# Performance work log

Measured on AMD Instinct MI355X. Metric: run time of the kernel, lower is better.

The kernel has to match this reference:

```python
import jax, jax.numpy as jnp
import numpy as np

WINDOW = (7, 7, 7)
DIM = 192
HEADS = 6
B_ = 256
NW = 32
N = int(np.prod(WINDOW))


def _relative_position_index(window_size):
    coords = np.stack(np.meshgrid(*[np.arange(w) for w in window_size], indexing='ij'))
    cf = coords.reshape(len(window_size), -1)  # (3, N)
    rel = cf[:, :, None] - cf[:, None, :]      # (3, N, N)
    rel = rel.transpose(1, 2, 0).copy()        # (N, N, 3)
    for i, w in enumerate(window_size):
        rel[:, :, i] += w - 1
    rel[:, :, 0] *= (2 * window_size[1] - 1) * (2 * window_size[2] - 1)
    rel[:, :, 1] *= 2 * window_size[2] - 1
    return rel.sum(-1).astype(np.int32)       # (N, N)


def setup_inputs() -> dict:
    key = jax.random.key(0)
    ks = jax.random.split(key, 8)
    table_rows = int(np.prod([2 * w - 1 for w in WINDOW]))  # 2197
    s = 0.02
    return {
        'skip': jax.random.normal(ks[0], (B_, N, DIM), jnp.float32),
        'x_up': jax.random.normal(ks[1], (B_, N, DIM), jnp.float32),
        'mask': jax.random.normal(ks[2], (NW, N, N), jnp.float32),
        'rel_index': jnp.asarray(_relative_position_index(WINDOW)),
        'table': s * jax.random.normal(ks[3], (table_rows, HEADS), jnp.float32),
        'kv_w': jax.random.normal(ks[4], (DIM, 2 * DIM), jnp.float32) / np.sqrt(DIM),
        'kv_b': jnp.zeros((2 * DIM,), jnp.float32),
        'proj_w': jax.random.normal(ks[5], (DIM, DIM), jnp.float32) / np.sqrt(DIM),
        'proj_b': jnp.zeros((DIM,), jnp.float32),
    }


def reference(skip, x_up, mask, rel_index, table, kv_w, kv_b, proj_w, proj_b):
    B, n, C = skip.shape
    H = HEADS
    D = C // H
    scale = D ** -0.5
    # kv projection: (B, N, 2C) -> k, v each (B, H, N, D)
    kv = skip @ kv_w + kv_b
    kv = kv.reshape(B, n, 2, H, D)
    k = kv[:, :, 0].transpose(0, 2, 1, 3)
    v = kv[:, :, 1].transpose(0, 2, 1, 3)
    q = (x_up.reshape(B, n, H, D).transpose(0, 2, 1, 3)) * scale
    attn = jnp.einsum('bhnd,bhmd->bhnm', q, k)  # (B, H, N, N)
    # gathered relative position bias: (N, N, H) -> (H, N, N)
    bias = table[rel_index].transpose(2, 0, 1)
    attn = attn + bias[None]
    nW = mask.shape[0]
    attn = attn.reshape(B // nW, nW, H, n, n) + mask[None, :, None]
    attn = jax.nn.softmax(attn.reshape(B, H, n, n), axis=-1)
    x = jnp.einsum('bhnm,bhmd->bhnd', attn, v)
    x = x.transpose(0, 2, 1, 3).reshape(B, n, C)
    return x @ proj_w + proj_b
```

## Files before the change

kernel.cpp:

```cpp
#include <hip/hip_runtime.h>
#include <hip/hip_bf16.h>

#define B_  256
#define N_  343
#define C_  192
#define H_  6
#define D_  32
#define NW_ 32
#define NN_ (N_*N_)
#define TROWS 2197
#define NP_ 352
#define PLANE (NP_*NP_)

typedef unsigned int  uint32;
typedef unsigned short u16;
typedef __attribute__((ext_vector_type(8))) short bf16x8;
typedef __attribute__((ext_vector_type(4))) float f32x4;

union frag8 { uint4 u4; bf16x8 h8; short s[8]; };

__device__ __forceinline__ float bf2f(u16 u){
  union { uint32 u; float f; } v; v.u = ((uint32)u) << 16; return v.f;
}
__device__ __forceinline__ u16 f2bf(float f){
  union { float f; uint32 u; } v; v.f = f;
  uint32 u = v.u;
  return (u16)((u + 0x7FFFu + ((u >> 16) & 1u)) >> 16);
}

__device__ __forceinline__ bool detect_f32(const uint32* w){
  int c = 0;
  #pragma unroll
  for (int u = 0; u < 32; u++){
    int e = (w[u*37] >> 7) & 0xFF;
    c += (e > 150);
  }
  return c >= 3;
}
__device__ __forceinline__ float ldf(const void* p, size_t i, bool f32){
  return f32 ? ((const float*)p)[i] : bf2f(((const u16*)p)[i]);
}
__device__ __forceinline__ void stf(void* p, size_t i, float v, bool f32){
  if (f32) ((float*)p)[i] = v;
  else     ((u16*)p)[i]   = f2bf(v);
}

__device__ __forceinline__ int klsidx(int j, int d){
  return j*32 + ((((d>>3) ^ ((j>>2)&3)))<<3) + (d&7);
}
__device__ __forceinline__ int vtidx(int d, int j){
  return d*352 + ((((j>>3) ^ ((d>>2)&3)))<<3) + (j&7);
}

__device__ __forceinline__ uint4 ld_row8(const void* __restrict__ src, bool F32,
                                         int b, int grow, int col){
  if (grow >= N_) return make_uint4(0,0,0,0);
  size_t g = ((size_t)b*N_ + grow)*C_ + col;
  if (F32){
    const float* gp = (const float*)src + g;
    float4 f0 = *(const float4*)gp, f1 = *(const float4*)(gp + 4);
    frag8 fv;
    fv.s[0]=(short)f2bf(f0.x); fv.s[1]=(short)f2bf(f0.y);
    fv.s[2]=(short)f2bf(f0.z); fv.s[3]=(short)f2bf(f0.w);
    fv.s[4]=(short)f2bf(f1.x); fv.s[5]=(short)f2bf(f1.y);
    fv.s[6]=(short)f2bf(f1.z); fv.s[7]=(short)f2bf(f1.w);
    return fv.u4;
  }
  return *(const uint4*)((const u16*)src + g);
}


__global__ void prep_bp(const void* __restrict__ skip, const int* __restrict__ rel,
                        const void* __restrict__ table, u16* __restrict__ bp){
  const bool F32 = detect_f32((const uint32*)skip);
  size_t gid = ((size_t)blockIdx.x*256 + threadIdx.x)*8;
  int p   = (int)(gid / PLANE);
  int rem = (int)(gid % PLANE);
  int i = rem / NP_, j0 = rem % NP_;
  frag8 o;
  #pragma unroll
  for (int m = 0; m < 8; m++){
    int j = j0 + m; float v = 0.f;
    if (i < N_ && j < N_){
      int r = rel[i*N_ + j];
      v = ldf(table, (size_t)r*H_ + p, F32);
    }
    o.s[m] = (short)f2bf(v);
  }
  *(uint4*)&bp[gid] = o.u4;
}

__global__ void prep_bm2(const void* __restrict__ skip, const void* __restrict__ mask,
                         const u16* __restrict__ bp, u16* __restrict__ bm){
  const bool F32 = detect_f32((const uint32*)skip);
  const float LOG2E = 1.4426950408889634f;
  size_t gid = ((size_t)blockIdx.x*256 + threadIdx.x)*8;
  int pl  = (int)(gid / PLANE);
  int rem = (int)(gid % PLANE);
  int i = rem / NP_, j0 = rem % NP_;
  int w = pl / H_, h = pl % H_;
  frag8 bg; bg.u4 = *(const uint4*)&bp[(size_t)h*PLANE + rem];
  frag8 o;
  #pragma unroll
  for (int m = 0; m < 8; m++){
    int j = j0 + m;
    float v = bf2f((u16)bg.s[m]);
    if (i < N_ && j < N_) v += ldf(mask, (size_t)w*NN_ + (size_t)i*N_ + j, F32);
    o.s[m] = (short)f2bf(v * LOG2E);
  }
  *(uint4*)&bm[gid] = o.u4;
}

__global__ __launch_bounds__(512, 2) void kv_gemm5(
    const void* __restrict__ skip, const void* __restrict__ kv_w,
    const void* __restrict__ kv_b, u16* __restrict__ kvws){
  __shared__ __align__(16) u16 sk[32*200];
  const bool F32 = detect_f32((const uint32*)skip);
  const int b = blockIdx.x;
  const int t = threadIdx.x, lane = t & 63, wave = t >> 6;
  const int n16 = lane & 15, q = lane >> 4;

  float kvb[3];
  u16*  p3[3];
  int   d3[3], isK[3];
  frag8 bw[3][6];
  #pragma unroll
  for (int c3 = 0; c3 < 3; c3++){
    int col = (wave*3 + c3)*16 + n16;
    kvb[c3] = ldf(kv_b, col, F32);
    #pragma unroll
    for (int ks = 0; ks < 6; ks++)
      #pragma unroll
      for (int j = 0; j < 8; j++)
        bw[c3][ks].s[j] = (short)f2bf(ldf(kv_w, (size_t)(ks*32 + q*8 + j)*384 + col, F32));
    if (col < 192){
      int h = col >> 5; d3[c3] = col & 31; isK[c3] = 1;
      p3[c3] = kvws + (size_t)(b*H_ + h)*22528;
    } else {
      int cv = col - 192; int h = cv >> 5; d3[c3] = cv & 31; isK[c3] = 0;
      p3[c3] = kvws + (size_t)(b*H_ + h)*22528 + 11264;
    }
  }

  const int r0 = t/24,        c0 = (t%24)*8;
  const int r1 = (t+512)/24,  c1 = ((t+512)%24)*8;
  const bool two = (t < 256);
  uint4 pre0 = ld_row8(skip, F32, b, r0, c0);
  uint4 pre1 = two ? ld_row8(skip, F32, b, r1, c1) : make_uint4(0,0,0,0);

  for (int rc = 0; rc < 11; rc++){
    __syncthreads();
    *(uint4*)&sk[r0*200 + c0] = pre0;
    if (two) *(uint4*)&sk[r1*200 + c1] = pre1;
    __syncthreads();
    if (rc < 10){
      int rb = (rc+1)*32;
      pre0 = ld_row8(skip, F32, b, rb + r0, c0);
      if (two) pre1 = ld_row8(skip, F32, b, rb + r1, c1);
    }
    frag8 af[2][6];
    #pragma unroll
    for (int half = 0; half < 2; half++)
      #pragma unroll
      for (int ks = 0; ks < 6; ks++)
        af[half][ks].u4 = *(const uint4*)&sk[(half*16 + n16)*200 + ks*32 + q*8];
    #pragma unroll
    for (int c3 = 0; c3 < 3; c3++){
      #pragma unroll
      for (int half = 0; half < 2; half++){
        f32x4 acc = {0.f,0.f,0.f,0.f};
        #pragma unroll
        for (int ks = 0; ks < 6; ks++)
          acc = __builtin_amdgcn_mfma_f32_16x16x32_bf16(af[half][ks].h8, bw[c3][ks].h8, acc, 0,0,0);
        #pragma unroll
        for (int r = 0; r < 4; r++){
          int grow = rc*32 + half*16 + q*4 + r;
          u16 val = f2bf(acc[r] + kvb[c3]);
          if (isK[c3]) p3[c3][klsidx(grow, d3[c3])] = val;
          else         p3[c3][vtidx(d3[c3], grow)] = val;
        }
      }
    }
  }
}

#define A2_VT  11264
#define A2_TOT 22528

__global__ __launch_bounds__(512, 6) void attn2(
    const void* __restrict__ skip, const void* __restrict__ x_up,
    const u16* __restrict__ bm, const u16* __restrict__ kvws,
    u16* __restrict__ xws, void* __restrict__ out){
  __shared__ __align__(16) u16 sm[A2_TOT];
  const bool F32 = detect_f32((const uint32*)skip);
  const int bid = blockIdx.x;
  const int b = bid / H_, h = bid % H_;
  const int w = b & (NW_-1);
  const int t = threadIdx.x, lane = t & 63, wave = t >> 6;
  const int n16 = lane & 15, q = lane >> 4;

  {
    const uint4* src = (const uint4*)(kvws + (size_t)bid*22528);
    uint4* dst = (uint4*)sm;
    for (int u = t; u < 2816; u += 512) dst[u] = src[u];
  }
  __syncthreads();

  const u16* bmp = bm + (size_t)(w*H_ + h)*PLANE;
  const float SC2 = 0.17677669529663687f * 1.4426950408889634f;

  for (int it = wave; it < 22; it += 8){
    int i0 = it*16;
    const u16* bmr = bmp + (size_t)(i0 + n16)*NP_;
    frag8 aq;
    {
      int qrow = min(i0 + n16, N_-1);
      size_t base = ((size_t)b*N_ + qrow)*C_ + h*D_ + q*8;
      if (F32){
        const float* xf = (const float*)x_up + base;
        float4 f0 = *(const float4*)xf, f1 = *(const float4*)(xf + 4);
        aq.s[0]=(short)f2bf(f0.x); aq.s[1]=(short)f2bf(f0.y);
        aq.s[2]=(short)f2bf(f0.z); aq.s[3]=(short)f2bf(f0.w);
        aq.s[4]=(short)f2bf(f1.x); aq.s[5]=(short)f2bf(f1.y);
        aq.s[6]=(short)f2bf(f1.z); aq.s[7]=(short)f2bf(f1.w);
      } else {
        aq.u4 = *(const uint4*)((const u16*)x_up + base);
      }
    }
    f32x4 O0 = {0.f,0.f,0.f,0.f}, O1 = {0.f,0.f,0.f,0.f};
    float lp = 0.f;
    for (int jc = 0; jc < 11; jc++){
      int j0 = jc*32;
      uint2 mba = *(const uint2*)&bmr[j0 + q*4];
      uint2 mbb = *(const uint2*)&bmr[j0 + 16 + q*4];
      frag8 bk0, bk1;
      bk0.u4 = *(const uint4*)&sm[klsidx(j0 + n16, q*8)];
      bk1.u4 = *(const uint4*)&sm[klsidx(j0 + 16 + n16, q*8)];
      f32x4 z = {0.f,0.f,0.f,0.f};
      f32x4 s0 = __builtin_amdgcn_mfma_f32_16x16x32_bf16(bk0.h8, aq.h8, z, 0,0,0);
      f32x4 s1 = __builtin_amdgcn_mfma_f32_16x16x32_bf16(bk1.h8, aq.h8, z, 0,0,0);
      union { uint2 v; u16 e[4]; } Ua, Ub;
      Ua.v = mba; Ub.v = mbb;
      float pa[4], pb[4];
      #pragma unroll
      for (int r = 0; r < 4; r++){
        pa[r] = exp2f(fmaf(s0[r], SC2, bf2f(Ua.e[r])));
        float eb = exp2f(fmaf(s1[r], SC2, bf2f(Ub.e[r])));
        pb[r] = (j0 + 16 + q*4 + r < N_) ? eb : 0.f;
        lp += pa[r] + pb[r];
      }
      uint32 A0, A1, B0, B1;
      asm("v_cvt_pk_bf16_f32 %0, %1, %2" : "=v"(A0) : "v"(pa[0]), "v"(pa[1]));
      asm("v_cvt_pk_bf16_f32 %0, %1, %2" : "=v"(A1) : "v"(pa[2]), "v"(pa[3]));
      asm("v_cvt_pk_bf16_f32 %0, %1, %2" : "=v"(B0) : "v"(pb[0]), "v"(pb[1]));
      asm("v_cvt_pk_bf16_f32 %0, %1, %2" : "=v"(B1) : "v"(pb[2]), "v"(pb[3]));
      int src0 = ((q & 1) << 5) + n16;
      int src1 = src0 + 16;
      uint32 a0s = (uint32)__shfl((int)A0, src0), a1s = (uint32)__shfl((int)A1, src0);
      uint32 a2s = (uint32)__shfl((int)A0, src1), a3s = (uint32)__shfl((int)A1, src1);
      uint32 b0s = (uint32)__shfl((int)B0, src0), b1s = (uint32)__shfl((int)B1, src0);
      uint32 b2s = (uint32)__shfl((int)B0, src1), b3s = (uint32)__shfl((int)B1, src1);
      bool lo = (q < 2);
      frag8 ap;
      ap.u4.x = lo ? a0s : b0s;
      ap.u4.y = lo ? a1s : b1s;
      ap.u4.z = lo ? a2s : b2s;
      ap.u4.w = lo ? a3s : b3s;
      frag8 bv0, bv1;
      bv0.u4 = *(const uint4*)&sm[A2_VT + vtidx(n16,      j0 + q*8)];
      bv1.u4 = *(const uint4*)&sm[A2_VT + vtidx(16 + n16, j0 + q*8)];
      O0 = __builtin_amdgcn_mfma_f32_16x16x32_bf16(ap.h8, bv0.h8, O0, 0,0,0);
      O1 = __builtin_amdgcn_mfma_f32_16x16x32_bf16(ap.h8, bv1.h8, O1, 0,0,0);
    }
    lp += __shfl_xor(lp, 16);
    lp += __shfl_xor(lp, 32);
    #pragma unroll
    for (int r = 0; r < 4; r++){
      int il = q*4 + r;
      float rl = 1.f / __shfl(lp, (lane & 48) | il);
      int i = i0 + il;
      if (i < N_){
        if (xws){
          u16* xp = xws + ((size_t)(b*H_ + h)*N_ + i)*D_;
          xp[n16]      = f2bf(O0[r]*rl);
          xp[16 + n16] = f2bf(O1[r]*rl);
        } else {
          size_t ob = ((size_t)b*N_ + i)*C_ + h*D_;
          stf(out, ob + n16,      O0[r]*rl, F32);
          stf(out, ob + 16 + n16, O1[r]*rl, F32);
        }
      }
    }
  }
}

__global__ __launch_bounds__(256, 4) void proj3(const u16* __restrict__ xws,
                                                void* __restrict__ outp,
                                                const void* __restrict__ pw,
                                                const void* __restrict__ pb,
                                                const void* __restrict__ skip){
  __shared__ __align__(16) u16 xs[64*200];
  const bool F32 = detect_f32((const uint32*)skip);
  const int t = threadIdx.x, lane = t & 63, wave = t >> 6;
  const int n16 = lane & 15, q = lane >> 4;
  const size_t row0 = (size_t)blockIdx.x * 64;

  for (int u = t; u < 1536; u += 256){
    int r = u / 24, c8 = u % 24;
    int g = (int)row0 + r;
    int b = g / N_, i = g - b*N_;
    int h = c8 >> 2, d0 = (c8 & 3)*8;
    uint4 vv = *(const uint4*)&xws[((size_t)(b*H_ + h)*N_ + i)*D_ + d0];
    *(uint4*)&xs[r*200 + h*32 + d0] = vv;
  }
  frag8 bwf[3][6];
  float pbv[3];
  #pragma unroll
  for (int c3 = 0; c3 < 3; c3++){
    int col = (wave*3 + c3)*16 + n16;
    pbv[c3] = ldf(pb, col, F32);
    #pragma unroll
    for (int ks = 0; ks < 6; ks++)
      #pragma unroll
      for (int j = 0; j < 8; j++)
        bwf[c3][ks].s[j] = (short)f2bf(ldf(pw, (size_t)(ks*32 + q*8 + j)*C_ + col, F32));
  }
  __syncthreads();
  for (int rt = 0; rt < 4; rt++){
    frag8 af[6];
    #pragma unroll
    for (int ks = 0; ks < 6; ks++)
      af[ks].u4 = *(const uint4*)&xs[(rt*16 + n16)*200 + ks*32 + q*8];
    #pragma unroll
    for (int c3 = 0; c3 < 3; c3++){
      f32x4 acc = {0.f,0.f,0.f,0.f};
      #pragma unroll
      for (int ks = 0; ks < 6; ks++)
        acc = __builtin_amdgcn_mfma_f32_16x16x32_bf16(af[ks].h8, bwf[c3][ks].h8, acc, 0,0,0);
      int col = (wave*3 + c3)*16 + n16;
      #pragma unroll
      for (int r = 0; r < 4; r++)
        stf(outp, (row0 + rt*16 + q*4 + r)*C_ + col, acc[r] + pbv[c3], F32);
    }
  }
}


__global__ void prep_biasg(const void* __restrict__ skip, const int* __restrict__ rel,
                           const void* __restrict__ table, u16* __restrict__ biasg){
  const bool F32 = detect_f32((const uint32*)skip);
  int idx = blockIdx.x*256 + threadIdx.x;
  if (idx >= NN_) return;
  int r = rel[idx];
  #pragma unroll
  for (int h = 0; h < H_; h++)
    biasg[(size_t)h*NN_ + idx] = f2bf(ldf(table, (size_t)r*H_ + h, F32));
}

#define KLS_OFF 6400
#define VT_OFF  (KLS_OFF + 352*40)
#define SMEM_U16 (VT_OFF + 32*360)

__global__ __launch_bounds__(512, 4) void attn_fused(
    const void* __restrict__ skip, const void* __restrict__ x_up,
    const void* __restrict__ mask, const u16* __restrict__ biasg,
    const void* __restrict__ kv_w, const void* __restrict__ kv_b,
    void* __restrict__ out){
  __shared__ __align__(16) u16 sm[SMEM_U16];
  const bool F32 = detect_f32((const uint32*)skip);
  const int bid = blockIdx.x;
  const int b = bid / H_, h = bid % H_;
  const int w = b & (NW_-1);
  const int t = threadIdx.x;
  const int lane = t & 63, wave = t >> 6;
  const int n16 = lane & 15, q = lane >> 4;
  const int colt = wave & 3;
  const int half = wave >> 2;
  const int gcol = (colt < 2) ? (h*D_ + colt*16 + n16)
                              : (C_ + h*D_ + (colt-2)*16 + n16);
  const float kvb = ldf(kv_b, gcol, F32);
  frag8 bw[6];
  #pragma unroll
  for (int ks = 0; ks < 6; ks++)
    #pragma unroll
    for (int j = 0; j < 8; j++)
      bw[ks].s[j] = (short)f2bf(ldf(kv_w, (size_t)(ks*32 + q*8 + j)*384 + gcol, F32));

  for (int rc = 0; rc < 11; rc++){
    __syncthreads();
    for (int u = t; u < 32*C_; u += 512){
      int r = u / C_, c = u % C_;
      int grow = rc*32 + r;
      float v = (grow < N_) ? ldf(skip, ((size_t)b*N_ + grow)*C_ + c, F32) : 0.f;
      sm[r*200 + c] = f2bf(v);
    }
    __syncthreads();
    f32x4 acc = {0.f, 0.f, 0.f, 0.f};
    #pragma unroll
    for (int ks = 0; ks < 6; ks++){
      frag8 a;  a.u4 = *(const uint4*)&sm[(half*16 + n16)*200 + ks*32 + q*8];
      acc = __builtin_amdgcn_mfma_f32_16x16x32_bf16(a.h8, bw[ks].h8, acc, 0, 0, 0);
    }
    #pragma unroll
    for (int r = 0; r < 4; r++){
      int grow = rc*32 + half*16 + q*4 + r;
      u16 val = f2bf(acc[r] + kvb);
      if (colt < 2) sm[KLS_OFF + grow*40 + colt*16 + n16] = val;
      else          sm[VT_OFF + ((colt-2)*16 + n16)*360 + grow] = val;
    }
  }
  __syncthreads();

  const float scale = 0.17677669529663687f;
  const size_t mwb = (size_t)w*NN_;
  const u16* bg = biasg + (size_t)h*NN_;
  u16* pls = &sm[wave*640];
  for (int it = wave; it < 22; it += 8){
    int i0 = it*16;
    {
      int rrow = min(i0 + (lane >> 2), N_-1);
      int col0 = (lane & 3)*8;
      size_t gb = ((size_t)b*N_ + rrow)*C_ + h*D_ + col0;
      u16* dst = &pls[(lane >> 2)*40 + col0];
      #pragma unroll
      for (int m = 0; m < 8; m++) dst[m] = f2bf(ldf(x_up, gb + m, F32) * scale);
    }
    frag8 aq; aq.u4 = *(const uint4*)&pls[n16*40 + q*8];
    f32x4 O0 = {0.f,0.f,0.f,0.f}, O1 = {0.f,0.f,0.f,0.f};
    float lp[4] = {0.f, 0.f, 0.f, 0.f};
    int ic[4];
    #pragma unroll
    for (int r = 0; r < 4; r++) ic[r] = min(i0 + q*4 + r, N_-1);
    for (int jc = 0; jc < 11; jc++){
      int j0 = jc*32;
      int ja = j0 + n16, jb = j0 + 16 + n16;
      int jac = min(ja, N_-1), jbc = min(jb, N_-1);
      float bma[4], bmb[4];
      #pragma unroll
      for (int r = 0; r < 4; r++){
        size_t rb = (size_t)ic[r]*N_;
        bma[r] = bf2f(bg[rb + jac]) + ldf(mask, mwb + rb + jac, F32);
        bmb[r] = bf2f(bg[rb + jbc]) + ldf(mask, mwb + rb + jbc, F32);
      }
      frag8 bk0, bk1;
      bk0.u4 = *(const uint4*)&sm[KLS_OFF + (j0 + n16)*40 + q*8];
      bk1.u4 = *(const uint4*)&sm[KLS_OFF + (j0 + 16 + n16)*40 + q*8];
      f32x4 z = {0.f,0.f,0.f,0.f};
      f32x4 s0 = __builtin_amdgcn_mfma_f32_16x16x32_bf16(aq.h8, bk0.h8, z, 0,0,0);
      f32x4 s1 = __builtin_amdgcn_mfma_f32_16x16x32_bf16(aq.h8, bk1.h8, z, 0,0,0);
      #pragma unroll
      for (int r = 0; r < 4; r++){
        float pa = (ja < N_) ? __expf(s0[r] + bma[r] - 12.f) : 0.f;
        float pb = (jb < N_) ? __expf(s1[r] + bmb[r] - 12.f) : 0.f;
        lp[r] += pa + pb;
        pls[(q*4 + r)*40 + n16]      = f2bf(pa);
        pls[(q*4 + r)*40 + 16 + n16] = f2bf(pb);
      }
      frag8 ap; ap.u4 = *(const uint4*)&pls[n16*40 + q*8];
      frag8 bv0, bv1;
      bv0.u4 = *(const uint4*)&sm[VT_OFF + n16*360 + j0 + q*8];
      bv1.u4 = *(const uint4*)&sm[VT_OFF + (16 + n16)*360 + j0 + q*8];
      O0 = __builtin_amdgcn_mfma_f32_16x16x32_bf16(ap.h8, bv0.h8, O0, 0,0,0);
      O1 = __builtin_amdgcn_mfma_f32_16x16x32_bf16(ap.h8, bv1.h8, O1, 0,0,0);
    }
    #pragma unroll
    for (int msk = 1; msk < 16; msk <<= 1){
      #pragma unroll
      for (int r = 0; r < 4; r++) lp[r] += __shfl_xor(lp[r], msk, 64);
    }
    #pragma unroll
    for (int r = 0; r < 4; r++){
      int i = i0 + q*4 + r;
      if (i < N_){
        float rl = 1.f / lp[r];
        size_t ob = ((size_t)b*N_ + i)*C_ + h*D_;
        stf(out, ob + n16,      O0[r]*rl, F32);
        stf(out, ob + 16 + n16, O1[r]*rl, F32);
      }
    }
  }
}

__global__ __launch_bounds__(256, 6) void proj2(void* __restrict__ io,
                                                const void* __restrict__ pw,
                                                const void* __restrict__ pb,
                                                const void* __restrict__ skip){
  __shared__ __align__(16) u16 xs[64*200];
  const bool F32 = detect_f32((const uint32*)skip);
  const int t = threadIdx.x;
  const int lane = t & 63, wave = t >> 6;
  const int n16 = lane & 15, q = lane >> 4;
  const size_t row0 = (size_t)blockIdx.x * 64;

  for (int u = t; u < 64*C_/8; u += 256){
    int r = u / 24, c = (u % 24)*8;
    size_t g = (row0 + r)*C_ + c;
    uint4 vv;
    if (F32){
      const float* gp = (const float*)io + g;
      float4 f0 = *(const float4*)gp, f1 = *(const float4*)(gp + 4);
      frag8 fv;
      fv.s[0]=(short)f2bf(f0.x); fv.s[1]=(short)f2bf(f0.y);
      fv.s[2]=(short)f2bf(f0.z); fv.s[3]=(short)f2bf(f0.w);
      fv.s[4]=(short)f2bf(f1.x); fv.s[5]=(short)f2bf(f1.y);
      fv.s[6]=(short)f2bf(f1.z); fv.s[7]=(short)f2bf(f1.w);
      vv = fv.u4;
    } else {
      vv = *(const uint4*)((const u16*)io + g);
    }
    *(uint4*)&xs[r*200 + c] = vv;
  }
  __syncthreads();
  for (int c3 = 0; c3 < 3; c3++){
    int col = (wave*3 + c3)*16 + n16;
    float pbv = ldf(pb, col, F32);
    frag8 bwf[6];
    #pragma unroll
    for (int ks = 0; ks < 6; ks++)
      #pragma unroll
      for (int j = 0; j < 8; j++)
        bwf[ks].s[j] = (short)f2bf(ldf(pw, (size_t)(ks*32 + q*8 + j)*C_ + col, F32));
    for (int rt = 0; rt < 4; rt++){
      frag8 af[6];
      #pragma unroll
      for (int ks = 0; ks < 6; ks++)
        af[ks].u4 = *(const uint4*)&xs[(rt*16 + n16)*200 + ks*32 + q*8];
      f32x4 acc = {0.f,0.f,0.f,0.f};
      #pragma unroll
      for (int ks = 0; ks < 6; ks++)
        acc = __builtin_amdgcn_mfma_f32_16x16x32_bf16(af[ks].h8, bwf[ks].h8, acc, 0,0,0);
      #pragma unroll
      for (int r = 0; r < 4; r++)
        stf(io, (row0 + rt*16 + q*4 + r)*C_ + col, acc[r] + pbv, F32);
    }
  }
}

extern "C" void kernel_launch(void* const* d_in, const int* in_sizes, int n_in,
                              void* d_out, int out_size, void* d_ws, size_t ws_size,
                              hipStream_t stream){
  (void)in_sizes; (void)n_in; (void)out_size;
  const void* skip  = d_in[0];
  const void* x_up  = d_in[1];
  const void* mask  = d_in[2];
  const int*  rel   = (const int*)d_in[3];
  const void* table = d_in[4];
  const void* kv_w  = d_in[5];
  const void* kv_b  = d_in[6];
  const void* pw    = d_in[7];
  const void* pb    = d_in[8];

  const size_t BM_BYTES = (size_t)192*PLANE*2;
  const size_t KV_BYTES = (size_t)B_*H_*45056;
  const size_t BP_BYTES = (size_t)H_*PLANE*2;
  const size_t XW_BYTES = (size_t)B_*H_*N_*D_*2;

  if (ws_size >= BM_BYTES + KV_BYTES + XW_BYTES){
    u16* bm   = (u16*)d_ws;
    u16* kvws = (u16*)((char*)d_ws + BM_BYTES);
    u16* xws  = (u16*)((char*)d_ws + BM_BYTES + KV_BYTES);
    u16* bp   = xws;
    prep_bp <<<(H_*PLANE/8)/256, 256, 0, stream>>>(skip, rel, table, bp);
    prep_bm2<<<(192*PLANE/8)/256, 256, 0, stream>>>(skip, mask, bp, bm);
    kv_gemm5<<<B_, 512, 0, stream>>>(skip, kv_w, kv_b, kvws);
    attn2   <<<B_*H_, 512, 0, stream>>>(skip, x_up, bm, kvws, xws, d_out);
    proj3   <<<87808/64, 256, 0, stream>>>(xws, d_out, pw, pb, skip);
  } else if (ws_size >= BM_BYTES + KV_BYTES + BP_BYTES){
    u16* bm   = (u16*)d_ws;
    u16* kvws = (u16*)((char*)d_ws + BM_BYTES);
    u16* bp   = (u16*)((char*)d_ws + BM_BYTES + KV_BYTES);
    prep_bp <<<(H_*PLANE/8)/256, 256, 0, stream>>>(skip, rel, table, bp);
    prep_bm2<<<(192*PLANE/8)/256, 256, 0, stream>>>(skip, mask, bp, bm);
    kv_gemm5<<<B_, 512, 0, stream>>>(skip, kv_w, kv_b, kvws);
    attn2   <<<B_*H_, 512, 0, stream>>>(skip, x_up, bm, kvws, nullptr, d_out);
    proj2   <<<87808/64, 256, 0, stream>>>(d_out, pw, pb, skip);
  } else {
    u16* biasg = (u16*)d_ws;
    prep_biasg<<<(NN_+255)/256, 256, 0, stream>>>(skip, rel, table, biasg);
    attn_fused<<<B_*H_, 512, 0, stream>>>(skip, x_up, mask, biasg, kv_w, kv_b, d_out);
    proj2     <<<87808/64, 256, 0, stream>>>(d_out, pw, pb, skip);
  }
}
```

Before: 449.6 us.

## Fuse bias/mask prep into kv projection kernel and peel masked softmax chunk

Merges the two bias-preparation kernels into extra blocks of the kv projection kernel, so the bias+mask plane is computed in one pass directly from table, rel_index and mask, with no intermediate bias plane. This removes two kernel launches and the intermediate buffer traffic, and lets the bias work overlap with the GEMM blocks. The attention inner loop also peels the last key chunk so bounds masking happens only there, and hoists the shuffle indices out of the loop. Launch bounds change to four blocks per CU, which may constrain registers for the GEMM path. The gather from table is now repeated for all 32 window planes instead of once per head.

```diff
diff --git a/kernel.cpp b/kernel.cpp
--- a/kernel.cpp
+++ b/kernel.cpp
@@ -70,54 +70,42 @@
 }
 
 
-__global__ void prep_bp(const void* __restrict__ skip, const int* __restrict__ rel,
-                        const void* __restrict__ table, u16* __restrict__ bp){
-  const bool F32 = detect_f32((const uint32*)skip);
-  size_t gid = ((size_t)blockIdx.x*256 + threadIdx.x)*8;
-  int p   = (int)(gid / PLANE);
-  int rem = (int)(gid % PLANE);
-  int i = rem / NP_, j0 = rem % NP_;
-  frag8 o;
-  #pragma unroll
-  for (int m = 0; m < 8; m++){
-    int j = j0 + m; float v = 0.f;
-    if (i < N_ && j < N_){
-      int r = rel[i*N_ + j];
-      v = ldf(table, (size_t)r*H_ + p, F32);
-    }
-    o.s[m] = (short)f2bf(v);
-  }
-  *(uint4*)&bp[gid] = o.u4;
-}
-
-__global__ void prep_bm2(const void* __restrict__ skip, const void* __restrict__ mask,
-                         const u16* __restrict__ bp, u16* __restrict__ bm){
-  const bool F32 = detect_f32((const uint32*)skip);
-  const float LOG2E = 1.4426950408889634f;
-  size_t gid = ((size_t)blockIdx.x*256 + threadIdx.x)*8;
-  int pl  = (int)(gid / PLANE);
-  int rem = (int)(gid % PLANE);
-  int i = rem / NP_, j0 = rem % NP_;
-  int w = pl / H_, h = pl % H_;
-  frag8 bg; bg.u4 = *(const uint4*)&bp[(size_t)h*PLANE + rem];
-  frag8 o;
-  #pragma unroll
-  for (int m = 0; m < 8; m++){
-    int j = j0 + m;
-    float v = bf2f((u16)bg.s[m]);
-    if (i < N_ && j < N_) v += ldf(mask, (size_t)w*NN_ + (size_t)i*N_ + j, F32);
-    o.s[m] = (short)f2bf(v * LOG2E);
-  }
-  *(uint4*)&bm[gid] = o.u4;
-}
-
-__global__ __launch_bounds__(512, 2) void kv_gemm5(
+#define BM_BLKS ((192*PLANE/8 + 511)/512)
+
+__global__ __launch_bounds__(512, 4) void kv_bm(
     const void* __restrict__ skip, const void* __restrict__ kv_w,
-    const void* __restrict__ kv_b, u16* __restrict__ kvws){
+    const void* __restrict__ kv_b, u16* __restrict__ kvws,
+    const int* __restrict__ rel, const void* __restrict__ table,
+    const void* __restrict__ mask, u16* __restrict__ bm){
   __shared__ __align__(16) u16 sk[32*200];
   const bool F32 = detect_f32((const uint32*)skip);
-  const int b = blockIdx.x;
-  const int t = threadIdx.x, lane = t & 63, wave = t >> 6;
+  const int bx = blockIdx.x;
+  const int t = threadIdx.x;
+
+  if (bx >= B_){
+    const float LOG2E = 1.4426950408889634f;
+    size_t gid = ((size_t)(bx - B_)*512 + t)*8;
+    int pl  = (int)(gid / PLANE);
+    int rem = (int)(gid % PLANE);
+    int i = rem / NP_, j0 = rem % NP_;
+    int w = pl / H_, h = pl % H_;
+    frag8 o;
+    #pragma unroll
+    for (int m = 0; m < 8; m++){
+      int j = j0 + m; float v = 0.f;
+      if (i < N_ && j < N_){
+        int r = rel[i*N_ + j];
+        v = (ldf(table, (size_t)r*H_ + h, F32)
+           + ldf(mask, (size_t)w*NN_ + (size_t)i*N_ + j, F32)) * LOG2E;
+      }
+      o.s[m] = (short)f2bf(v);
+    }
+    *(uint4*)&bm[gid] = o.u4;
+    return;
+  }
+
+  const int b = bx;
+  const int lane = t & 63, wave = t >> 6;
   const int n16 = lane & 15, q = lane >> 4;
 
   float kvb[3];
@@ -208,6 +196,9 @@
 
   const u16* bmp = bm + (size_t)(w*H_ + h)*PLANE;
   const float SC2 = 0.17677669529663687f * 1.4426950408889634f;
+  const int src0 = ((q & 1) << 5) + n16;
+  const int src1 = src0 + 16;
+  const bool lo = (q < 2);
 
   for (int it = wave; it < 22; it += 8){
     int i0 = it*16;
@@ -242,25 +233,31 @@
       union { uint2 v; u16 e[4]; } Ua, Ub;
       Ua.v = mba; Ub.v = mbb;
       float pa[4], pb[4];
-      #pragma unroll
-      for (int r = 0; r < 4; r++){
-        pa[r] = exp2f(fmaf(s0[r], SC2, bf2f(Ua.e[r])));
-        float eb = exp2f(fmaf(s1[r], SC2, bf2f(Ub.e[r])));
-        pb[r] = (j0 + 16 + q*4 + r < N_) ? eb : 0.f;
-        lp += pa[r] + pb[r];
+      if (jc < 10){
+        #pragma unroll
+        for (int r = 0; r < 4; r++){
+          pa[r] = exp2f(fmaf(s0[r], SC2, bf2f(Ua.e[r])));
+          pb[r] = exp2f(fmaf(s1[r], SC2, bf2f(Ub.e[r])));
+          lp += pa[r] + pb[r];
+        }
+      } else {
+        #pragma unroll
+        for (int r = 0; r < 4; r++){
+          pa[r] = exp2f(fmaf(s0[r], SC2, bf2f(Ua.e[r])));
+          float eb = exp2f(fmaf(s1[r], SC2, bf2f(Ub.e[r])));
+          pb[r] = (336 + q*4 + r < N_) ? eb : 0.f;
+          lp += pa[r] + pb[r];
+        }
       }
       uint32 A0, A1, B0, B1;
       asm("v_cvt_pk_bf16_f32 %0, %1, %2" : "=v"(A0) : "v"(pa[0]), "v"(pa[1]));
       asm("v_cvt_pk_bf16_f32 %0, %1, %2" : "=v"(A1) : "v"(pa[2]), "v"(pa[3]));
       asm("v_cvt_pk_bf16_f32 %0, %1, %2" : "=v"(B0) : "v"(pb[0]), "v"(pb[1]));
       asm("v_cvt_pk_bf16_f32 %0, %1, %2" : "=v"(B1) : "v"(pb[2]), "v"(pb[3]));
-      int src0 = ((q & 1) << 5) + n16;
-      int src1 = src0 + 16;
       uint32 a0s = (uint32)__shfl((int)A0, src0), a1s = (uint32)__shfl((int)A1, src0);
       uint32 a2s = (uint32)__shfl((int)A0, src1), a3s = (uint32)__shfl((int)A1, src1);
       uint32 b0s = (uint32)__shfl((int)B0, src0), b1s = (uint32)__shfl((int)B1, src0);
       uint32 b2s = (uint32)__shfl((int)B0, src1), b3s = (uint32)__shfl((int)B1, src1);
-      bool lo = (q < 2);
       frag8 ap;
       ap.u4.x = lo ? a0s : b0s;
       ap.u4.y = lo ? a1s : b1s;
@@ -552,28 +549,21 @@
 
   const size_t BM_BYTES = (size_t)192*PLANE*2;
   const size_t KV_BYTES = (size_t)B_*H_*45056;
-  const size_t BP_BYTES = (size_t)H_*PLANE*2;
   const size_t XW_BYTES = (size_t)B_*H_*N_*D_*2;
 
   if (ws_size >= BM_BYTES + KV_BYTES + XW_BYTES){
     u16* bm   = (u16*)d_ws;
     u16* kvws = (u16*)((char*)d_ws + BM_BYTES);
     u16* xws  = (u16*)((char*)d_ws + BM_BYTES + KV_BYTES);
-    u16* bp   = xws;
-    prep_bp <<<(H_*PLANE/8)/256, 256, 0, stream>>>(skip, rel, table, bp);
-    prep_bm2<<<(192*PLANE/8)/256, 256, 0, stream>>>(skip, mask, bp, bm);
-    kv_gemm5<<<B_, 512, 0, stream>>>(skip, kv_w, kv_b, kvws);
-    attn2   <<<B_*H_, 512, 0, stream>>>(skip, x_up, bm, kvws, xws, d_out);
-    proj3   <<<87808/64, 256, 0, stream>>>(xws, d_out, pw, pb, skip);
-  } else if (ws_size >= BM_BYTES + KV_BYTES + BP_BYTES){
+    kv_bm<<<B_ + BM_BLKS, 512, 0, stream>>>(skip, kv_w, kv_b, kvws, rel, table, mask, bm);
+    attn2<<<B_*H_, 512, 0, stream>>>(skip, x_up, bm, kvws, xws, d_out);
+    proj3<<<87808/64, 256, 0, stream>>>(xws, d_out, pw, pb, skip);
+  } else if (ws_size >= BM_BYTES + KV_BYTES){
     u16* bm   = (u16*)d_ws;
     u16* kvws = (u16*)((char*)d_ws + BM_BYTES);
-    u16* bp   = (u16*)((char*)d_ws + BM_BYTES + KV_BYTES);
-    prep_bp <<<(H_*PLANE/8)/256, 256, 0, stream>>>(skip, rel, table, bp);
-    prep_bm2<<<(192*PLANE/8)/256, 256, 0, stream>>>(skip, mask, bp, bm);
-    kv_gemm5<<<B_, 512, 0, stream>>>(skip, kv_w, kv_b, kvws);
-    attn2   <<<B_*H_, 512, 0, stream>>>(skip, x_up, bm, kvws, nullptr, d_out);
-    proj2   <<<87808/64, 256, 0, stream>>>(d_out, pw, pb, skip);
+    kv_bm<<<B_ + BM_BLKS, 512, 0, stream>>>(skip, kv_w, kv_b, kvws, rel, table, mask, bm);
+    attn2<<<B_*H_, 512, 0, stream>>>(skip, x_up, bm, kvws, nullptr, d_out);
+    proj2<<<87808/64, 256, 0, stream>>>(d_out, pw, pb, skip);
   } else {
     u16* biasg = (u16*)d_ws;
     prep_biasg<<<(NN_+255)/256, 256, 0, stream>>>(skip, rel, table, biasg);
```

After: 572.8 us. 27.4% more time.
